# Performance work log

Hardware: AMD Instinct MI355X
Metric: run time of the kernel (lower is better)

The kernel has to match this reference:

```python
import jax, jax.numpy as jnp
import numpy as np

T, D, E, K = 16384, 4096, 64, 8
GUMBEL_TAU = 1.0
ROUTER_TEMP = 1.0
SELECT_TEMP = None  # falls back to router_temp, as in the module
EPS = 1e-06


def setup_inputs() -> dict:
    key = jax.random.key(0)
    k1, k2, k3 = jax.random.split(key, 3)
    h = jax.random.normal(k1, (T, D), dtype=jnp.float32)
    # eqx.nn.Linear weight: shape (out_features, in_features), uniform init scale
    W = jax.random.normal(k2, (E, D), dtype=jnp.float32) * (1.0 / np.sqrt(D))
    # uniform noise for Gumbel, matching minval=1e-6, maxval=1-1e-6
    u = jax.random.uniform(k3, (T, E), minval=EPS, maxval=1.0 - EPS, dtype=jnp.float32)
    return {"h": h, "W": W, "u": u}


def reference(h, W, u):
    # logits_clean = vmap(Linear)(h) = h @ W.T, shape (T, E)
    logits_clean = jnp.einsum("td,ed->te", h, W)

    t_mix = jnp.clip(jnp.float32(ROUTER_TEMP), EPS, None)
    probs = jax.nn.softmax(logits_clean / t_mix, axis=-1)

    sel_temp = ROUTER_TEMP if SELECT_TEMP is None else SELECT_TEMP
    t_sel = jnp.clip(jnp.float32(sel_temp), EPS, None)
    logits_sel = logits_clean / t_sel

    # training path: Gumbel noise g = -log(-log(u))
    g = -jnp.log(-jnp.log(u))
    logits_sel = logits_sel + GUMBEL_TAU * g

    # hard top-k mask per row (scatter of ones at top-k indices == one_hot().sum())
    _, idx = jax.lax.top_k(logits_sel, K)  # (T, K)
    rows = jnp.arange(logits_sel.shape[0])[:, None]
    mask_full = jnp.zeros(logits_sel.shape, dtype=bool).at[rows, idx].set(True)

    return (mask_full, probs, logits_clean, logits_sel)
```

## Files before the change

kernel.cpp:

```cpp
#include <hip/hip_runtime.h>
#include <hip/hip_bf16.h>
#include <math.h>
#include <stdint.h>

#define T_ROWS 16384
#define D_DIM  4096
#define E_EXP  64
#define TOPK   8

constexpr float W_SCALE   = 64.0f;
constexpr float INV_SCALE = 1.0f / 64.0f;

constexpr int BM   = 32;
constexpr int BK   = 64;
constexpr int NIT  = D_DIM / BK;
constexpr int ABUF = 8192;
constexpr int BBUF = 16384;
constexpr int B_OFF = 3 * ABUF;
constexpr int LDS_TOT = B_OFF + 3 * BBUF;

typedef _Float16 f16x8 __attribute__((ext_vector_type(8)));
typedef __fp16   h16x2 __attribute__((ext_vector_type(2)));
typedef float    f32x4 __attribute__((ext_vector_type(4)));

__device__ __forceinline__ void gll16(const void* g, void* l) {
    __builtin_amdgcn_global_load_lds(
        (const __attribute__((address_space(1))) void*)g,
        (__attribute__((address_space(3))) void*)l, 16, 0, 0);
}
#define WAITV(n) asm volatile("s_waitcnt vmcnt(" #n ")" ::: "memory")
#define SB0()    __builtin_amdgcn_sched_barrier(0)

__global__ __launch_bounds__(256) void wprep_kernel(
    const float* __restrict__ W, _Float16* __restrict__ Whi,
    _Float16* __restrict__ Wlo)
{
    const int i  = blockIdx.x * 256 + threadIdx.x;
    const int e  = i >> 9;
    const int k8 = i & 511;
    const int k  = k8 << 3;
    const int t  = k >> 6;
    const int s  = (k >> 3) & 7;
    const float4 w0 = *(const float4*)&W[(size_t)e * D_DIM + k];
    const float4 w1 = *(const float4*)&W[(size_t)e * D_DIM + k + 4];
    const float xs[8] = {w0.x, w0.y, w0.z, w0.w, w1.x, w1.y, w1.z, w1.w};
    f16x8 hi, lo;
    #pragma unroll
    for (int j = 0; j < 8; ++j) {
        const float x = xs[j] * W_SCALE;
        const _Float16 hh = (_Float16)x;
        hi[j] = hh;
        lo[j] = (_Float16)(x - (float)hh);
    }
    const size_t o = (size_t)t * 4096 + e * 64 + ((s ^ (e & 7)) << 3);
    *(f16x8*)(Whi + o) = hi;
    *(f16x8*)(Wlo + o) = lo;
}

__device__ __forceinline__ void cvt8(const float4 x0, const float4 x1,
                                     f16x8& hi, f16x8& lo) {
    const float xs[8] = {x0.x, x0.y, x0.z, x0.w, x1.x, x1.y, x1.z, x1.w};
    float hs[8], ls[8];
    #pragma unroll
    for (int j = 0; j < 8; ++j) {
        hs[j] = __uint_as_float(__float_as_uint(xs[j]) & 0xFFFFE000u);
        ls[j] = xs[j] - hs[j];
    }
    #pragma unroll
    for (int j = 0; j < 4; ++j) {
        const h16x2 ph = __builtin_amdgcn_cvt_pkrtz(hs[2 * j], hs[2 * j + 1]);
        const h16x2 pl = __builtin_amdgcn_cvt_pkrtz(ls[2 * j], ls[2 * j + 1]);
        hi[2 * j] = (_Float16)ph[0]; hi[2 * j + 1] = (_Float16)ph[1];
        lo[2 * j] = (_Float16)pl[0]; lo[2 * j + 1] = (_Float16)pl[1];
    }
}

__global__ __launch_bounds__(256, 2) void router_main_kernel(
    const float* __restrict__ h, const _Float16* __restrict__ Whi,
    const _Float16* __restrict__ Wlo, const float* __restrict__ u,
    float* __restrict__ out)
{
    __shared__ union {
        char raw[LDS_TOT];
        float logits[BM][E_EXP + 4];
    } sm;
    char* smb = sm.raw;

    const int tid  = threadIdx.x;
    const int wv   = tid >> 6;
    const int lane = tid & 63;
    const int l15  = lane & 15;
    const int kg   = lane >> 4;
    const int wm   = wv >> 1;
    const int we   = wv & 1;
    const int row0 = blockIdx.x * BM;

    const char* gA[2]; int lA[2];
    #pragma unroll
    for (int p = 0; p < 2; ++p) {
        const int j   = wv * 2 + p;
        const int row = j * 4 + kg;
        gA[p] = (const char*)h + (size_t)(row0 + row) * (D_DIM * 4)
                + ((l15 ^ (row & 15)) << 4);
        lA[p] = j * 1024;
    }
    const char* gB[4]; int lB[4];
    #pragma unroll
    for (int q = 0; q < 4; ++q) {
        const int j = wv * 4 + q;
        const _Float16* src = (j < 8) ? Whi : Wlo;
        gB[q] = (const char*)src + (size_t)(j & 7) * 1024 + lane * 16;
        lB[q] = B_OFF + j * 1024;
    }

    int aro[2][2];
    #pragma unroll
    for (int kc = 0; kc < 2; ++kc)
        #pragma unroll
        for (int q2 = 0; q2 < 2; ++q2)
            aro[kc][q2] = (wm * 16 + l15) * 256
                        + (((kc * 8 + kg * 2 + q2) ^ l15) << 4);
    int bro[2][2][2];
    #pragma unroll
    for (int sel = 0; sel < 2; ++sel)
        #pragma unroll
        for (int es = 0; es < 2; ++es)
            #pragma unroll
            for (int kc = 0; kc < 2; ++kc) {
                const int e = we * 32 + es * 16 + l15;
                bro[sel][es][kc] = B_OFF + sel * 8192 + e * 128
                                 + (((kc * 4 + kg) ^ (l15 & 7)) << 4);
            }

    f32x4 acc[2] = {};
    float4 av[2][2];
    f16x8 bhf[2][2], blf[2][2];

    int aCur = 0, aNxt = ABUF, aStg = 2 * ABUF;
    int bCur = 0, bNxt = BBUF, bStg = 2 * BBUF;

    #define STAGE(t, aAdd, bAdd)                                   \
        { _Pragma("unroll")                                        \
          for (int p = 0; p < 2; ++p)                              \
              gll16(gA[p] + (size_t)(t) * 256, smb + (aAdd) + lA[p]); \
          _Pragma("unroll")                                        \
          for (int q = 0; q < 4; ++q)                              \
              gll16(gB[q] + (size_t)(t) * 8192, smb + (bAdd) + lB[q]); }

    #define DSREAD(aAdd, bAdd)                                                \
        { _Pragma("unroll")                                                   \
          for (int kc = 0; kc < 2; ++kc)                                      \
              _Pragma("unroll")                                               \
              for (int q2 = 0; q2 < 2; ++q2)                                  \
                  av[kc][q2] = *(const float4*)(smb + (aAdd) + aro[kc][q2]);  \
          _Pragma("unroll")                                                   \
          for (int es = 0; es < 2; ++es)                                      \
              _Pragma("unroll")                                               \
              for (int kc = 0; kc < 2; ++kc) {                                \
                  bhf[es][kc] = *(const f16x8*)(smb + (bAdd) + bro[0][es][kc]);\
                  blf[es][kc] = *(const f16x8*)(smb + (bAdd) + bro[1][es][kc]);\
              } }

    #define MFMAS()                                                           \
        { f16x8 ah[2], al[2];                                                 \
          cvt8(av[0][0], av[0][1], ah[0], al[0]);                             \
          cvt8(av[1][0], av[1][1], ah[1], al[1]);                             \
          _Pragma("unroll")                                                   \
          for (int es = 0; es < 2; ++es)                                      \
              _Pragma("unroll")                                               \
              for (int kc = 0; kc < 2; ++kc) {                                \
                  acc[es] = __builtin_amdgcn_mfma_f32_16x16x32_f16(ah[kc], bhf[es][kc], acc[es], 0, 0, 0); \
                  acc[es] = __builtin_amdgcn_mfma_f32_16x16x32_f16(ah[kc], blf[es][kc], acc[es], 0, 0, 0); \
                  acc[es] = __builtin_amdgcn_mfma_f32_16x16x32_f16(al[kc], bhf[es][kc], acc[es], 0, 0, 0); \
              } }

    #define ROT() { int t_;                                        \
        t_ = aCur; aCur = aNxt; aNxt = aStg; aStg = t_;            \
        t_ = bCur; bCur = bNxt; bNxt = bStg; bStg = t_; }

    STAGE(0, aCur, bCur)
    STAGE(1, aNxt, bNxt)
    WAITV(6);
    __builtin_amdgcn_s_barrier();

    for (int i = 0; i < NIT - 2; ++i) {
        DSREAD(aCur, bCur)
        STAGE(i + 2, aStg, bStg)
        SB0();
        __builtin_amdgcn_s_barrier();
        __builtin_amdgcn_s_setprio(1);
        MFMAS()
        __builtin_amdgcn_s_setprio(0);
        WAITV(6);
        SB0();
        __builtin_amdgcn_s_barrier();
        ROT();
    }
    DSREAD(aCur, bCur)
    __builtin_amdgcn_s_barrier();
    MFMAS()
    WAITV(0);
    SB0();
    __builtin_amdgcn_s_barrier();
    ROT();
    DSREAD(aCur, bCur)
    MFMAS()
    __builtin_amdgcn_s_barrier();

    #pragma unroll
    for (int es = 0; es < 2; ++es)
        #pragma unroll
        for (int r = 0; r < 4; ++r)
            sm.logits[wm * 16 + kg * 4 + r][we * 32 + es * 16 + l15]
                = acc[es][r] * INV_SCALE;
    __syncthreads();

    const size_t te = (size_t)T_ROWS * E_EXP;
    #pragma unroll
    for (int rr = 0; rr < 8; ++rr) {
        const int rl = wv * 8 + rr;
        const int gr = row0 + rl;
        const size_t idx = (size_t)gr * E_EXP + lane;
        const float val = sm.logits[rl][lane];

        out[2 * te + idx] = val;

        float m = val;
        #pragma unroll
        for (int off = 32; off; off >>= 1) m = fmaxf(m, __shfl_xor(m, off));
        const float p = expf(val - m);
        float ssum = p;
        #pragma unroll
        for (int off = 32; off; off >>= 1) ssum += __shfl_xor(ssum, off);
        out[1 * te + idx] = p / ssum;

        const float uv = u[idx];
        const float g = -logf(-logf(uv));
        const float sel = val + g;
        out[3 * te + idx] = sel;

        float v = sel;
        bool chosen = false;
        #pragma unroll
        for (int itk = 0; itk < TOPK; ++itk) {
            float mv = v;
            #pragma unroll
            for (int off = 32; off; off >>= 1) mv = fmaxf(mv, __shfl_xor(mv, off));
            const unsigned long long b = __ballot(v == mv);
            const int sl = __ffsll((long long)b) - 1;
            if (lane == sl) { chosen = true; v = -INFINITY; }
        }
        out[idx] = chosen ? 1.0f : 0.0f;
    }
}

extern "C" void kernel_launch(void* const* d_in, const int* in_sizes, int n_in,
                              void* d_out, int out_size, void* d_ws, size_t ws_size,
                              hipStream_t stream) {
    const float* h = (const float*)d_in[0];
    const float* W = (const float*)d_in[1];
    const float* u = (const float*)d_in[2];
    float* out = (float*)d_out;

    _Float16* Whi = (_Float16*)d_ws;
    _Float16* Wlo = Whi + (size_t)E_EXP * D_DIM;

    hipLaunchKernelGGL(wprep_kernel, dim3(E_EXP * D_DIM / 8 / 256), dim3(256),
                       0, stream, W, Whi, Wlo);
    hipLaunchKernelGGL(router_main_kernel, dim3(T_ROWS / BM), dim3(256),
                       0, stream, h, Whi, Wlo, u, out);
}
```

Before: 89.47 us.

## Split K across two blocks and move softmax/top-k to separate epilogue kernel

```diff
diff --git a/kernel.cpp b/kernel.cpp
--- a/kernel.cpp
+++ b/kernel.cpp
@@ -12,10 +12,11 @@
 constexpr float INV_SCALE = 1.0f / 64.0f;
 
 constexpr int BM   = 32;
-constexpr int BK   = 64;
-constexpr int NIT  = D_DIM / BK;
-constexpr int ABUF = 8192;
-constexpr int BBUF = 16384;
+constexpr int BK   = 32;
+constexpr int KHALF = D_DIM / 2;
+constexpr int NIT  = KHALF / BK;
+constexpr int ABUF = 4096;
+constexpr int BBUF = 8192;
 constexpr int B_OFF = 3 * ABUF;
 constexpr int LDS_TOT = B_OFF + 3 * BBUF;
 
@@ -32,15 +33,14 @@
 #define SB0()    __builtin_amdgcn_sched_barrier(0)
 
 __global__ __launch_bounds__(256) void wprep_kernel(
-    const float* __restrict__ W, _Float16* __restrict__ Whi,
-    _Float16* __restrict__ Wlo)
+    const float* __restrict__ W, _Float16* __restrict__ Wt)
 {
     const int i  = blockIdx.x * 256 + threadIdx.x;
     const int e  = i >> 9;
     const int k8 = i & 511;
     const int k  = k8 << 3;
-    const int t  = k >> 6;
-    const int s  = (k >> 3) & 7;
+    const int t  = k >> 5;
+    const int s  = (k >> 3) & 3;
     const float4 w0 = *(const float4*)&W[(size_t)e * D_DIM + k];
     const float4 w1 = *(const float4*)&W[(size_t)e * D_DIM + k + 4];
     const float xs[8] = {w0.x, w0.y, w0.z, w0.w, w1.x, w1.y, w1.z, w1.w};
@@ -52,9 +52,9 @@
         hi[j] = hh;
         lo[j] = (_Float16)(x - (float)hh);
     }
-    const size_t o = (size_t)t * 4096 + e * 64 + ((s ^ (e & 7)) << 3);
-    *(f16x8*)(Whi + o) = hi;
-    *(f16x8*)(Wlo + o) = lo;
+    const size_t o = (size_t)t * 4096 + e * 32 + ((s ^ (e & 3)) << 3);
+    *(f16x8*)(Wt + o) = hi;
+    *(f16x8*)(Wt + o + 2048) = lo;
 }
 
 __device__ __forceinline__ void cvt8(const float4 x0, const float4 x1,
@@ -75,16 +75,11 @@
     }
 }
 
-__global__ __launch_bounds__(256, 2) void router_main_kernel(
-    const float* __restrict__ h, const _Float16* __restrict__ Whi,
-    const _Float16* __restrict__ Wlo, const float* __restrict__ u,
+__global__ __launch_bounds__(256, 4) void gemm_half_kernel(
+    const float* __restrict__ h, const _Float16* __restrict__ Wt,
     float* __restrict__ out)
 {
-    __shared__ union {
-        char raw[LDS_TOT];
-        float logits[BM][E_EXP + 4];
-    } sm;
-    char* smb = sm.raw;
+    __shared__ char smb[LDS_TOT];
 
     const int tid  = threadIdx.x;
     const int wv   = tid >> 6;
@@ -94,93 +89,70 @@
     const int wm   = wv >> 1;
     const int we   = wv & 1;
     const int row0 = blockIdx.x * BM;
-
-    const char* gA[2]; int lA[2];
-    #pragma unroll
-    for (int p = 0; p < 2; ++p) {
-        const int j   = wv * 2 + p;
-        const int row = j * 4 + kg;
-        gA[p] = (const char*)h + (size_t)(row0 + row) * (D_DIM * 4)
-                + ((l15 ^ (row & 15)) << 4);
-        lA[p] = j * 1024;
-    }
-    const char* gB[4]; int lB[4];
-    #pragma unroll
-    for (int q = 0; q < 4; ++q) {
-        const int j = wv * 4 + q;
-        const _Float16* src = (j < 8) ? Whi : Wlo;
-        gB[q] = (const char*)src + (size_t)(j & 7) * 1024 + lane * 16;
-        lB[q] = B_OFF + j * 1024;
-    }
-
-    int aro[2][2];
-    #pragma unroll
-    for (int kc = 0; kc < 2; ++kc)
-        #pragma unroll
-        for (int q2 = 0; q2 < 2; ++q2)
-            aro[kc][q2] = (wm * 16 + l15) * 256
-                        + (((kc * 8 + kg * 2 + q2) ^ l15) << 4);
-    int bro[2][2][2];
+    const int by   = blockIdx.y;
+    const int kb   = by * KHALF;
+
+    const int arow = wv * 8 + (lane >> 3);
+    const char* gA = (const char*)h + ((size_t)(row0 + arow) * D_DIM + kb) * 4
+                     + (((lane & 7) ^ (arow & 7)) << 4);
+    const char* gB = (const char*)Wt + (size_t)by * 64 * 8192
+                     + wv * 2048 + lane * 16;
+    const int lB = B_OFF + wv * 2048;
+
+    int aro[2];
+    #pragma unroll
+    for (int q = 0; q < 2; ++q)
+        aro[q] = (wm * 16 + l15) * 128 + (((kg * 2 + q) ^ (l15 & 7)) << 4);
+    int bro[2][2];
     #pragma unroll
     for (int sel = 0; sel < 2; ++sel)
         #pragma unroll
-        for (int es = 0; es < 2; ++es)
-            #pragma unroll
-            for (int kc = 0; kc < 2; ++kc) {
-                const int e = we * 32 + es * 16 + l15;
-                bro[sel][es][kc] = B_OFF + sel * 8192 + e * 128
-                                 + (((kc * 4 + kg) ^ (l15 & 7)) << 4);
-            }
+        for (int es = 0; es < 2; ++es) {
+            const int e = we * 32 + es * 16 + l15;
+            bro[sel][es] = B_OFF + sel * 4096 + e * 64 + ((kg ^ (e & 3)) << 4);
+        }
 
     f32x4 acc[2] = {};
-    float4 av[2][2];
-    f16x8 bhf[2][2], blf[2][2];
+    float4 av[2];
+    f16x8 bhf[2], blf[2];
 
     int aCur = 0, aNxt = ABUF, aStg = 2 * ABUF;
     int bCur = 0, bNxt = BBUF, bStg = 2 * BBUF;
 
-    #define STAGE(t, aAdd, bAdd)                                   \
-        { _Pragma("unroll")                                        \
-          for (int p = 0; p < 2; ++p)                              \
-              gll16(gA[p] + (size_t)(t) * 256, smb + (aAdd) + lA[p]); \
-          _Pragma("unroll")                                        \
-          for (int q = 0; q < 4; ++q)                              \
-              gll16(gB[q] + (size_t)(t) * 8192, smb + (bAdd) + lB[q]); }
+    #define STAGE(t, aAdd, bAdd)                                      \
+        { gll16(gA + (size_t)(t) * 128, smb + (aAdd) + wv * 1024);    \
+          gll16(gB + (size_t)(t) * 8192,        smb + (bAdd) + lB);          \
+          gll16(gB + (size_t)(t) * 8192 + 1024, smb + (bAdd) + lB + 1024); }
 
     #define DSREAD(aAdd, bAdd)                                                \
-        { _Pragma("unroll")                                                   \
-          for (int kc = 0; kc < 2; ++kc)                                      \
-              _Pragma("unroll")                                               \
-              for (int q2 = 0; q2 < 2; ++q2)                                  \
-                  av[kc][q2] = *(const float4*)(smb + (aAdd) + aro[kc][q2]);  \
+        { av[0] = *(const float4*)(smb + (aAdd) + aro[0]);                    \
+          av[1] = *(const float4*)(smb + (aAdd) + aro[1]);                    \
           _Pragma("unroll")                                                   \
-          for (int es = 0; es < 2; ++es)                                      \
-              _Pragma("unroll")                                               \
-              for (int kc = 0; kc < 2; ++kc) {                                \
-                  bhf[es][kc] = *(const f16x8*)(smb + (bAdd) + bro[0][es][kc]);\
-                  blf[es][kc] = *(const f16x8*)(smb + (bAdd) + bro[1][es][kc]);\
-              } }
+          for (int es = 0; es < 2; ++es) {                                    \
+              bhf[es] = *(const f16x8*)(smb + (bAdd) + bro[0][es]);           \
+              blf[es] = *(const f16x8*)(smb + (bAdd) + bro[1][es]);           \
+          } }
 
     #define MFMAS()                                                           \
-        { f16x8 ah[2], al[2];                                                 \
-          cvt8(av[0][0], av[0][1], ah[0], al[0]);                             \
-          cvt8(av[1][0], av[1][1], ah[1], al[1]);                             \
+        { f16x8 ah, al;                                                       \
+          cvt8(av[0], av[1], ah, al);                                         \
           _Pragma("unroll")                                                   \
-          for (int es = 0; es < 2; ++es)                                      \
-              _Pragma("unroll")                                               \
-              for (int kc = 0; kc < 2; ++kc) {                                \
-                  acc[es] = __builtin_amdgcn_mfma_f32_16x16x32_f16(ah[kc], bhf[es][kc], acc[es], 0, 0, 0); \
-                  acc[es] = __builtin_amdgcn_mfma_f32_16x16x32_f16(ah[kc], blf[es][kc], acc[es], 0, 0, 0); \
-                  acc[es] = __builtin_amdgcn_mfma_f32_16x16x32_f16(al[kc], bhf[es][kc], acc[es], 0, 0, 0); \
-              } }
+          for (int es = 0; es < 2; ++es) {                                    \
+              acc[es] = __builtin_amdgcn_mfma_f32_16x16x32_f16(ah, bhf[es], acc[es], 0, 0, 0); \
+              acc[es] = __builtin_amdgcn_mfma_f32_16x16x32_f16(ah, blf[es], acc[es], 0, 0, 0); \
+              acc[es] = __builtin_amdgcn_mfma_f32_16x16x32_f16(al, bhf[es], acc[es], 0, 0, 0); \
+          } }
 
     #define ROT() { int t_;                                        \
         t_ = aCur; aCur = aNxt; aNxt = aStg; aStg = t_;            \
         t_ = bCur; bCur = bNxt; bNxt = bStg; bStg = t_; }
 
     STAGE(0, aCur, bCur)
+    SB0();
     STAGE(1, aNxt, bNxt)
-    WAITV(6);
+    SB0();
+    WAITV(3);
+    SB0();
     __builtin_amdgcn_s_barrier();
 
     for (int i = 0; i < NIT - 2; ++i) {
@@ -191,7 +163,7 @@
         __builtin_amdgcn_s_setprio(1);
         MFMAS()
         __builtin_amdgcn_s_setprio(0);
-        WAITV(6);
+        WAITV(3);
         SB0();
         __builtin_amdgcn_s_barrier();
         ROT();
@@ -205,53 +177,56 @@
     ROT();
     DSREAD(aCur, bCur)
     MFMAS()
-    __builtin_amdgcn_s_barrier();
-
+
+    float* slot = out + (size_t)(2 + by) * T_ROWS * E_EXP;
     #pragma unroll
     for (int es = 0; es < 2; ++es)
         #pragma unroll
         for (int r = 0; r < 4; ++r)
-            sm.logits[wm * 16 + kg * 4 + r][we * 32 + es * 16 + l15]
-                = acc[es][r] * INV_SCALE;
-    __syncthreads();
-
+            slot[(size_t)(row0 + wm * 16 + kg * 4 + r) * E_EXP
+                 + we * 32 + es * 16 + l15] = acc[es][r];
+}
+
+__global__ __launch_bounds__(256) void epilogue_kernel(
+    const float* __restrict__ u, float* __restrict__ out)
+{
+    const int row  = blockIdx.x * 4 + (threadIdx.x >> 6);
+    const int lane = threadIdx.x & 63;
     const size_t te = (size_t)T_ROWS * E_EXP;
-    #pragma unroll
-    for (int rr = 0; rr < 8; ++rr) {
-        const int rl = wv * 8 + rr;
-        const int gr = row0 + rl;
-        const size_t idx = (size_t)gr * E_EXP + lane;
-        const float val = sm.logits[rl][lane];
-
-        out[2 * te + idx] = val;
-
-        float m = val;
+    const size_t idx = (size_t)row * E_EXP + lane;
+
+    const float p0 = out[2 * te + idx];
+    const float p1 = out[3 * te + idx];
+    const float val = (p0 + p1) * INV_SCALE;
+
+    out[2 * te + idx] = val;
+
+    float m = val;
+    #pragma unroll
+    for (int off = 32; off; off >>= 1) m = fmaxf(m, __shfl_xor(m, off));
+    const float p = expf(val - m);
+    float ssum = p;
+    #pragma unroll
+    for (int off = 32; off; off >>= 1) ssum += __shfl_xor(ssum, off);
+    out[1 * te + idx] = p / ssum;
+
+    const float uv = u[idx];
+    const float g = -logf(-logf(uv));
+    const float sel = val + g;
+    out[3 * te + idx] = sel;
+
+    float v = sel;
+    bool chosen = false;
+    #pragma unroll
+    for (int itk = 0; itk < TOPK; ++itk) {
+        float mv = v;
         #pragma unroll
-        for (int off = 32; off; off >>= 1) m = fmaxf(m, __shfl_xor(m, off));
-        const float p = expf(val - m);
-        float ssum = p;
-        #pragma unroll
-        for (int off = 32; off; off >>= 1) ssum += __shfl_xor(ssum, off);
-        out[1 * te + idx] = p / ssum;
-
-        const float uv = u[idx];
-        const float g = -logf(-logf(uv));
-        const float sel = val + g;
-        out[3 * te + idx] = sel;
-
-        float v = sel;
-        bool chosen = false;
-        #pragma unroll
-        for (int itk = 0; itk < TOPK; ++itk) {
-            float mv = v;
-            #pragma unroll
-            for (int off = 32; off; off >>= 1) mv = fmaxf(mv, __shfl_xor(mv, off));
-            const unsigned long long b = __ballot(v == mv);
-            const int sl = __ffsll((long long)b) - 1;
-            if (lane == sl) { chosen = true; v = -INFINITY; }
-        }
-        out[idx] = chosen ? 1.0f : 0.0f;
-    }
+        for (int off = 32; off; off >>= 1) mv = fmaxf(mv, __shfl_xor(mv, off));
+        const unsigned long long b = __ballot(v == mv);
+        const int sl = __ffsll((long long)b) - 1;
+        if (lane == sl) { chosen = true; v = -INFINITY; }
+    }
+    out[idx] = chosen ? 1.0f : 0.0f;
 }
 
 extern "C" void kernel_launch(void* const* d_in, const int* in_sizes, int n_in,
@@ -262,11 +237,12 @@
     const float* u = (const float*)d_in[2];
     float* out = (float*)d_out;
 
-    _Float16* Whi = (_Float16*)d_ws;
-    _Float16* Wlo = Whi + (size_t)E_EXP * D_DIM;
+    _Float16* Wt = (_Float16*)d_ws;
 
     hipLaunchKernelGGL(wprep_kernel, dim3(E_EXP * D_DIM / 8 / 256), dim3(256),
-                       0, stream, W, Whi, Wlo);
-    hipLaunchKernelGGL(router_main_kernel, dim3(T_ROWS / BM), dim3(256),
-                       0, stream, h, Whi, Wlo, u, out);
-}
+                       0, stream, W, Wt);
+    hipLaunchKernelGGL(gemm_half_kernel, dim3(T_ROWS / BM, 2), dim3(256),
+                       0, stream, h, Wt, out);
+    hipLaunchKernelGGL(epilogue_kernel, dim3(T_ROWS / 4), dim3(256),
+                       0, stream, u, out);
+}
```

Result: faster. 86.33 us (-3.5%).
